# Kernel tuning notes

Hardware: AMD Instinct MI355X
Metric: run time of the kernel (lower is better)

The kernel has to match this reference:

```python
import jax, jax.numpy as jnp
import numpy as np

N_HEAD = 16
LN_EPS = 1e-5


def _layernorm(x, g, b):
    mu = jnp.mean(x, axis=-1, keepdims=True)
    var = jnp.mean(jnp.square(x - mu), axis=-1, keepdims=True)
    return (x - mu) * jax.lax.rsqrt(var + LN_EPS) * g + b


def setup_inputs() -> dict:
    key = jax.random.key(0)
    ks = jax.random.split(key, 8)
    B, T, C = 2, 2048, 1024
    Dff = 4 * C
    s = 0.02
    return {
        "x": jax.random.normal(ks[0], (B, T, C), jnp.float32),
        "wq": jax.random.normal(ks[1], (C, C), jnp.float32) * s,
        "wk": jax.random.normal(ks[2], (C, C), jnp.float32) * s,
        "wv": jax.random.normal(ks[3], (C, C), jnp.float32) * s,
        "w_proj": jax.random.normal(ks[4], (C, C), jnp.float32) * s,
        "b_proj": jnp.zeros((C,), jnp.float32),
        "w1": jax.random.normal(ks[5], (C, Dff), jnp.float32) * s,
        "b1": jnp.zeros((Dff,), jnp.float32),
        "w2": jax.random.normal(ks[6], (Dff, C), jnp.float32) * s,
        "b2": jnp.zeros((C,), jnp.float32),
        "g1": jnp.ones((C,), jnp.float32),
        "be1": jnp.zeros((C,), jnp.float32),
        "g2": jnp.ones((C,), jnp.float32),
        "be2": jnp.zeros((C,), jnp.float32),
    }


def reference(x, wq, wk, wv, w_proj, b_proj, w1, b1, w2, b2, g1, be1, g2, be2):
    B, T, C = x.shape
    H = N_HEAD
    hd = C // H
    # QKV projections (all heads folded into one matmul each), -> [B,H,T,hd]
    q = (x @ wq).reshape(B, T, H, hd).transpose(0, 2, 1, 3)
    k = (x @ wk).reshape(B, T, H, hd).transpose(0, 2, 1, 3)
    v = (x @ wv).reshape(B, T, H, hd).transpose(0, 2, 1, 3)
    # scaled causal attention; scale = head_size ** -0.5 as in torch source
    scores = jnp.einsum("bhqd,bhkd->bhqk", q, k) * (hd ** -0.5)
    causal = jnp.tril(jnp.ones((T, T), bool))
    scores = jnp.where(causal, scores, jnp.finfo(scores.dtype).min)
    wei = jax.nn.softmax(scores, axis=-1)
    attn = jnp.einsum("bhqk,bhkd->bhqd", wei, v)  # [B,H,T,hd]
    attn = attn.transpose(0, 2, 1, 3).reshape(B, T, C)
    y = attn @ w_proj + b_proj
    # post-LN residuals as in Block.forward
    x = _layernorm(x + y, g1, be1)
    y = jnp.maximum(x @ w1 + b1, 0.0) @ w2 + b2
    x = _layernorm(x + y, g2, be2)
    return x
```

## Files before the change

### kernel.cpp

```cpp
#include <hip/hip_runtime.h>
#include <hip/hip_bf16.h>


typedef __attribute__((ext_vector_type(8))) short bf16x8;
typedef __attribute__((ext_vector_type(4))) float f32x4;
typedef __attribute__((ext_vector_type(4))) short short4v;

__device__ inline short f2bf(float f) {
    __hip_bfloat16 h = __float2bfloat16(f);
    return *reinterpret_cast<short*>(&h);
}
__device__ inline float bf2f(short s) {
    union { unsigned u; float f; } c;
    c.u = ((unsigned)(unsigned short)s) << 16;
    return c.f;
}


__global__ __launch_bounds__(256) void convert_f2b(const float* __restrict__ in,
                                                   short* __restrict__ out, int n4) {
    int i = blockIdx.x * 256 + threadIdx.x;
    if (i < n4) {
        float4 v = *(const float4*)(in + (size_t)i * 4);
        short4v o = { f2bf(v.x), f2bf(v.y), f2bf(v.z), f2bf(v.w) };
        *(short4v*)(out + (size_t)i * 4) = o;
    }
}

__global__ __launch_bounds__(256) void transpose4_f2b(const float* __restrict__ s0,
                                                      const float* __restrict__ s1,
                                                      const float* __restrict__ s2,
                                                      const float* __restrict__ s3,
                                                      short* __restrict__ d0,
                                                      short* __restrict__ d1,
                                                      short* __restrict__ d2,
                                                      short* __restrict__ d3,
                                                      float scale0) {
    __shared__ short tile[32][33];
    const int z = blockIdx.z;
    const float* in = z == 0 ? s0 : z == 1 ? s1 : z == 2 ? s2 : s3;
    short* out = z == 0 ? d0 : z == 1 ? d1 : z == 2 ? d2 : d3;
    const float scale = z == 0 ? scale0 : 1.0f;
    int c0 = blockIdx.x * 32, r0 = blockIdx.y * 32;
    int tx = threadIdx.x, ty = threadIdx.y;
    for (int i = ty; i < 32; i += 8)
        tile[i][tx] = f2bf(in[(size_t)(r0 + i) * 1024 + c0 + tx] * scale);
    __syncthreads();
    for (int i = ty; i < 32; i += 8)
        out[(size_t)(c0 + i) * 1024 + r0 + tx] = tile[tx][i];
}

__global__ __launch_bounds__(256) void transpose_f2b(const float* __restrict__ in,
                                                     short* __restrict__ out, int R, int C,
                                                     float scale) {
    __shared__ short tile[32][33];
    int c0 = blockIdx.x * 32, r0 = blockIdx.y * 32;
    int tx = threadIdx.x, ty = threadIdx.y;
    for (int i = ty; i < 32; i += 8)
        tile[i][tx] = f2bf(in[(size_t)(r0 + i) * C + c0 + tx] * scale);
    __syncthreads();
    for (int i = ty; i < 32; i += 8)
        out[(size_t)(c0 + i) * R + r0 + tx] = tile[tx][i];
}

template <int BN, int BIAS, int RELU, int OUTBF>
__device__ __forceinline__ void gemm_core(const short* __restrict__ A,
                                          const short* __restrict__ BT,
                                          const float* __restrict__ bias,
                                          void* __restrict__ Cout,
                                          int N, int K, int lda, int ldb,
                                          int gx, int w,
                                          short* As, short* Bs, bool addbias) {
    constexpr int NI = BN / 32;
    const int tid = threadIdx.x;
    const int wid = tid >> 6;
    const int lane = tid & 63;
    const int wr = wid >> 1, wc = wid & 1;
    const int row0 = (w % gx) * 128;
    const int col0 = (w / gx) * BN;
    const int lr = lane & 15;
    const int lk = (lane >> 4) * 8;
    const int sr = lane >> 3;
    const int scs = ((lane & 7) * 8) ^ (sr * 8);
    const int rsw = (lr & 7) * 8;

    f32x4 acc[4][NI] = {};
    for (int k = 0; k < K; k += 64) {
#pragma unroll
        for (int c = 0; c < 4; ++c) {
            const int ch = wid + c * 4;
            const short* ga = A + (size_t)(row0 + ch * 8 + sr) * lda + k + scs;
            __builtin_amdgcn_global_load_lds(
                (const __attribute__((address_space(1))) unsigned int*)ga,
                (__attribute__((address_space(3))) unsigned int*)(As + ch * 512), 16, 0, 0);
        }
#pragma unroll
        for (int c = 0; c < BN / 32; ++c) {
            const int ch = wid + c * 4;
            const short* gb = BT + (size_t)(col0 + ch * 8 + sr) * ldb + k + scs;
            __builtin_amdgcn_global_load_lds(
                (const __attribute__((address_space(1))) unsigned int*)gb,
                (__attribute__((address_space(3))) unsigned int*)(Bs + ch * 512), 16, 0, 0);
        }
        __syncthreads();
#pragma unroll
        for (int kk = 0; kk < 64; kk += 32) {
            const int cof = (kk + lk) ^ rsw;
            bf16x8 a[4], b[NI];
#pragma unroll
            for (int m = 0; m < 4; ++m)
                a[m] = *(const bf16x8*)(As + (wr * 64 + m * 16 + lr) * 64 + cof);
#pragma unroll
            for (int n = 0; n < NI; ++n)
                b[n] = *(const bf16x8*)(Bs + (wc * (BN / 2) + n * 16 + lr) * 64 + cof);
#pragma unroll
            for (int m = 0; m < 4; ++m)
#pragma unroll
                for (int n = 0; n < NI; ++n)
                    acc[m][n] = __builtin_amdgcn_mfma_f32_16x16x32_bf16(a[m], b[n], acc[m][n], 0, 0, 0);
        }
        __syncthreads();
    }
#pragma unroll
    for (int m = 0; m < 4; ++m) {
        int row = row0 + wr * 64 + m * 16 + (lane >> 4) * 4;
#pragma unroll
        for (int n = 0; n < NI; ++n) {
            int col = col0 + wc * (BN / 2) + n * 16 + lr;
            float bv = (BIAS && addbias) ? bias[col] : 0.0f;
#pragma unroll
            for (int r = 0; r < 4; ++r) {
                float v = acc[m][n][r] + bv;
                if (RELU) v = fmaxf(v, 0.0f);
                if (OUTBF)
                    ((short*)Cout)[(size_t)(row + r) * N + col] = f2bf(v);
                else
                    ((float*)Cout)[(size_t)(row + r) * N + col] = v;
            }
        }
    }
}

template <int BN, int BIAS, int RELU, int OUTBF>
__global__ __launch_bounds__(256) void gemm_bt(const short* __restrict__ A,
                                               const short* __restrict__ BT,
                                               const float* __restrict__ bias,
                                               void* __restrict__ Cout,
                                               int N, int K, int lda, int ldb,
                                               void* __restrict__ Cout2) {
    __shared__ short As[128 * 64];
    __shared__ short Bs[BN * 64];
    const int kz = blockIdx.z;
    if (kz) { A += K; BT += K; Cout = Cout2; }
    const int gx = gridDim.x;
    int flat = blockIdx.x + gx * blockIdx.y;
    const int nwg = gx * gridDim.y;
    int w = flat;
    if ((nwg & 7) == 0) {
        const int q = nwg >> 3;
        w = (flat & 7) * q + (flat >> 3);
    }
    gemm_core<BN, BIAS, RELU, OUTBF>(A, BT, bias, Cout, N, K, lda, ldb, gx, w, As, Bs, kz == 0);
}

__global__ __launch_bounds__(256) void gemm_qkv_vt(const short* __restrict__ x_bf,
                                                   const short* __restrict__ wqkT,
                                                   const short* __restrict__ wvT,
                                                   short* __restrict__ qk,
                                                   short* __restrict__ Vt) {
    __shared__ short As[128 * 64];
    __shared__ short Bs[128 * 64];
    int flat = blockIdx.x;
    if (flat < 512) {
        const int w = (flat & 7) * 64 + (flat >> 3);
        gemm_core<128, 0, 0, 1>(x_bf, wqkT, nullptr, qk, 2048, 1024, 1024, 1024, 32, w, As, Bs, false);
    } else {
        flat -= 512;
        const int w = (flat & 7) * 32 + (flat >> 3);
        gemm_core<128, 0, 0, 1>(wvT, x_bf, nullptr, Vt, 4096, 1024, 1024, 1024, 8, w, As, Bs, false);
    }
}

#define ATT_T 2048
#define ATT_QKS 2048
#define ATT_BT 4096

#define LOADK(KF, KB)                                                                     \
    do {                                                                                  \
        const int k0_ = (KB) * 64;                                                        \
        _Pragma("unroll") for (int t = 0; t < 4; ++t) {                                   \
            const size_t krow_ = (size_t)(b * ATT_T + k0_ + 16 * t + lr) * ATT_QKS + h * 64; \
            KF[t][0] = *(const bf16x8*)(Km + krow_ + g * 8);                              \
            KF[t][1] = *(const bf16x8*)(Km + krow_ + 32 + g * 8);                         \
        }                                                                                 \
    } while (0)

#define LOADV(VF, KB)                                                                     \
    do {                                                                                  \
        const int k0_ = (KB) * 64;                                                        \
        _Pragma("unroll") for (int n = 0; n < 4; ++n)                                     \
            _Pragma("unroll") for (int ks = 0; ks < 2; ++ks)                              \
                VF[n][ks] = *(const bf16x8*)(Vt + (size_t)(h * 64 + n * 16 + lr) * ATT_BT + \
                                             b * ATT_T + k0_ + ks * 32 + g * 8);          \
    } while (0)

#define COMPUTE(KF, VF, KB)                                                               \
    do {                                                                                  \
        const int k0_ = (KB) * 64;                                                        \
        const bool edge_ = (KB) == nfull;                                                 \
        _Pragma("unroll") for (int qs = 0; qs < 2; ++qs) {                                \
            f32x4 st[4];                                                                  \
            __builtin_amdgcn_s_setprio(1);                                                \
            _Pragma("unroll") for (int t = 0; t < 4; ++t) {                               \
                f32x4 s = {};                                                             \
                s = __builtin_amdgcn_mfma_f32_16x16x32_bf16(KF[t][0], aq[qs][0], s, 0, 0, 0); \
                s = __builtin_amdgcn_mfma_f32_16x16x32_bf16(KF[t][1], aq[qs][1], s, 0, 0, 0); \
                st[t] = s;                                                                \
            }                                                                             \
            __builtin_amdgcn_s_setprio(0);                                                \
            float rs = 0.0f;                                                              \
            _Pragma("unroll") for (int t = 0; t < 4; ++t) {                               \
                short4v pw;                                                               \
                _Pragma("unroll") for (int r = 0; r < 4; ++r) {                           \
                    float val = st[t][r];                                                 \
                    if (edge_ && (k0_ + 16 * t + g * 4 + r > qrow[qs])) val = -3e38f;     \
                    float p = exp2f(val);                                                 \
                    rs += p;                                                              \
                    pw[r] = f2bf(p);                                                      \
                }                                                                         \
                *(short4v*)(&Plds[wid][qs][lr][16 * t + g * 4]) = pw;                     \
            }                                                                             \
            rs += __shfl_xor(rs, 16);                                                     \
            rs += __shfl_xor(rs, 32);                                                     \
            lrun[qs] += rs;                                                               \
        }                                                                                 \
        asm volatile("s_waitcnt lgkmcnt(0)" ::: "memory");                                \
        __builtin_amdgcn_sched_barrier(0);                                                \
        __builtin_amdgcn_s_setprio(1);                                                    \
        _Pragma("unroll") for (int qs = 0; qs < 2; ++qs)                                  \
            _Pragma("unroll") for (int ks = 0; ks < 2; ++ks) {                            \
                bf16x8 pf = *(const bf16x8*)(&Plds[wid][qs][lr][ks * 32 + g * 8]);        \
                _Pragma("unroll") for (int n = 0; n < 4; ++n)                             \
                    O[qs][n] = __builtin_amdgcn_mfma_f32_16x16x32_bf16(VF[n][ks], pf, O[qs][n], 0, 0, 0); \
            }                                                                             \
        __builtin_amdgcn_s_setprio(0);                                                    \
    } while (0)

__global__ __launch_bounds__(128) void flash_attn(const short* __restrict__ Q,
                                                  const short* __restrict__ Km,
                                                  const short* __restrict__ Vt,
                                                  short* __restrict__ Oout) {
    const int f = blockIdx.x;
    const int wid = threadIdx.x >> 6;
    const int lane = threadIdx.x & 63;
    const int lr = lane & 15;
    const int g = lane >> 4;
    const int xcd = f & 7;
    const int k = f >> 3;
    const int bh = xcd * 4 + (k & 3);
    const int b = bh >> 4;
    const int h = bh & 15;
    const int pair = (k >> 2) * 2 + wid;

    __shared__ __align__(16) short Plds[2][2][16][72];

#pragma unroll 1
    for (int job = 0; job < 2; ++job) {
        const int s = job ? (63 - pair) : pair;
        const int q0 = s << 5;
        const int qrow[2] = { q0 + lr, q0 + 16 + lr };
        const int nfull = s >> 1;

        bf16x8 aq[2][2];
#pragma unroll
        for (int qs = 0; qs < 2; ++qs)
#pragma unroll
            for (int ds = 0; ds < 2; ++ds)
                aq[qs][ds] = *(const bf16x8*)(Q + (size_t)(b * ATT_T + q0 + qs * 16 + lr) * ATT_QKS +
                                              h * 64 + ds * 32 + g * 8);

        f32x4 O[2][4] = {};
        float lrun[2] = { 0.0f, 0.0f };

        bf16x8 kfA[4][2], kfB[4][2], vfA[4][2], vfB[4][2];
        LOADK(kfA, 0);
        LOADV(vfA, 0);
        int kb = 0;
        while (true) {
            if (kb < nfull) { LOADK(kfB, kb + 1); LOADV(vfB, kb + 1); }
            COMPUTE(kfA, vfA, kb);
            ++kb;
            if (kb > nfull) break;
            if (kb < nfull) { LOADK(kfA, kb + 1); LOADV(vfA, kb + 1); }
            COMPUTE(kfB, vfB, kb);
            ++kb;
            if (kb > nfull) break;
        }

#pragma unroll
        for (int qs = 0; qs < 2; ++qs) {
            const float inv = 1.0f / lrun[qs];
#pragma unroll
            for (int n = 0; n < 4; ++n) {
                short4v ov;
#pragma unroll
                for (int r = 0; r < 4; ++r) ov[r] = f2bf(O[qs][n][r] * inv);
                *(short4v*)(Oout + (size_t)(b * ATT_T + q0 + qs * 16 + lr) * 1024 +
                            h * 64 + n * 16 + g * 4) = ov;
            }
        }
    }
}

__global__ __launch_bounds__(256) void resid_ln(const float* __restrict__ x,
                                                const short* __restrict__ y,
                                                const short* __restrict__ yb,
                                                const float* __restrict__ g,
                                                const float* __restrict__ be,
                                                float* __restrict__ of,
                                                short* __restrict__ ob) {
    const int row = blockIdx.x;
    const int tid = threadIdx.x;
    const size_t base = (size_t)row * 1024 + tid * 4;
    float4 xv = *(const float4*)(x + base);
    short4v yv = *(const short4v*)(y + base);
    float h0 = xv.x + bf2f(yv[0]), h1 = xv.y + bf2f(yv[1]);
    float h2 = xv.z + bf2f(yv[2]), h3 = xv.w + bf2f(yv[3]);
    if (yb) {
        short4v bv2 = *(const short4v*)(yb + base);
        h0 += bf2f(bv2[0]); h1 += bf2f(bv2[1]); h2 += bf2f(bv2[2]); h3 += bf2f(bv2[3]);
    }
    float s = h0 + h1 + h2 + h3;
    float ss = h0 * h0 + h1 * h1 + h2 * h2 + h3 * h3;
#pragma unroll
    for (int d = 1; d < 64; d <<= 1) {
        s += __shfl_xor(s, d);
        ss += __shfl_xor(ss, d);
    }
    __shared__ float as_[4], ass_[4];
    if ((tid & 63) == 0) { as_[tid >> 6] = s; ass_[tid >> 6] = ss; }
    __syncthreads();
    s = as_[0] + as_[1] + as_[2] + as_[3];
    ss = ass_[0] + ass_[1] + ass_[2] + ass_[3];
    const float mu = s * (1.0f / 1024.0f);
    const float var = ss * (1.0f / 1024.0f) - mu * mu;
    const float rstd = rsqrtf(var + 1e-5f);
    float4 gv = *(const float4*)(g + tid * 4);
    float4 bv = *(const float4*)(be + tid * 4);
    float o0 = (h0 - mu) * rstd * gv.x + bv.x;
    float o1 = (h1 - mu) * rstd * gv.y + bv.y;
    float o2 = (h2 - mu) * rstd * gv.z + bv.z;
    float o3 = (h3 - mu) * rstd * gv.w + bv.w;
    float4 ov = { o0, o1, o2, o3 };
    *(float4*)(of + base) = ov;
    if (ob) {
        short4v obv = { f2bf(o0), f2bf(o1), f2bf(o2), f2bf(o3) };
        *(short4v*)(ob + base) = obv;
    }
}


extern "C" void kernel_launch(void* const* d_in, const int* in_sizes, int n_in,
                              void* d_out, int out_size, void* d_ws, size_t ws_size,
                              hipStream_t stream) {
    const float* x = (const float*)d_in[0];
    const float* wq = (const float*)d_in[1];
    const float* wk = (const float*)d_in[2];
    const float* wv = (const float*)d_in[3];
    const float* wp = (const float*)d_in[4];
    const float* bproj = (const float*)d_in[5];
    const float* w1 = (const float*)d_in[6];
    const float* b1 = (const float*)d_in[7];
    const float* w2 = (const float*)d_in[8];
    const float* b2 = (const float*)d_in[9];
    const float* g1 = (const float*)d_in[10];
    const float* be1 = (const float*)d_in[11];
    const float* g2 = (const float*)d_in[12];
    const float* be2 = (const float*)d_in[13];

    char* ws = (char*)d_ws;
    const size_t MB = 1024 * 1024;
    short* x_bf = (short*)(ws + 0);
    short* wqkT = (short*)(ws + 8 * MB);
    short* wqT = wqkT;
    short* wkT = (short*)(ws + 10 * MB);
    short* wvT = (short*)(ws + 12 * MB);
    short* w1T = (short*)(ws + 16 * MB);
    short* w2T = (short*)(ws + 24 * MB);
    short* qk  = (short*)(ws + 32 * MB);
    short* wpT = (short*)(ws + 48 * MB);
    short* Vt  = (short*)(ws + 56 * MB);
    short* hbf = (short*)(ws + 32 * MB);
    short* attn = (short*)(ws + 64 * MB);
    short* x1bf = (short*)(ws + 64 * MB);
    short* y1a = (short*)(ws + 72 * MB);
    short* y1b = (short*)(ws + 0);
    short* y2a = (short*)(ws + 72 * MB);
    short* y2b = (short*)(ws + 0);
    float* x1f = (float*)(ws + 88 * MB);

    dim3 blk(256);
    dim3 tb(32, 8);
    const float SC = 0.125f * 1.44269504089f;

    convert_f2b<<<dim3(4096), blk, 0, stream>>>(x, x_bf, 4096 * 1024 / 4);
    transpose4_f2b<<<dim3(32, 32, 4), tb, 0, stream>>>(wq, wk, wv, wp, wqT, wkT, wvT, wpT, SC);
    transpose_f2b<<<dim3(128, 32), tb, 0, stream>>>(w1, w1T, 1024, 4096, 1.0f);
    transpose_f2b<<<dim3(32, 128), tb, 0, stream>>>(w2, w2T, 4096, 1024, 1.0f);

    gemm_qkv_vt<<<dim3(768), blk, 0, stream>>>(x_bf, wqkT, wvT, qk, Vt);
    flash_attn<<<dim3(512), dim3(128), 0, stream>>>(qk, qk + 1024, Vt, attn);
    gemm_bt<64, 1, 0, 1><<<dim3(32, 16, 2), blk, 0, stream>>>(attn, wpT, bproj, y1a,
                                                              1024, 512, 1024, 1024, y1b);
    resid_ln<<<dim3(4096), blk, 0, stream>>>(x, y1a, y1b, g1, be1, x1f, x1bf);
    gemm_bt<128, 1, 1, 1><<<dim3(32, 32), blk, 0, stream>>>(x1bf, w1T, b1, hbf,
                                                            4096, 1024, 1024, 1024, nullptr);
    gemm_bt<64, 1, 0, 1><<<dim3(32, 16, 2), blk, 0, stream>>>(hbf, w2T, b2, y2a,
                                                              1024, 2048, 4096, 4096, y2b);
    resid_ln<<<dim3(4096), blk, 0, stream>>>(x1f, y2a, y2b, g2, be2, (float*)d_out, nullptr);
}
```

Baseline: 295.4 us.

## Merge prep conversion kernels into one launch and single-buffer V in attention

The x conversion and all the weight transpose/convert kernels are folded into one mega_prep launch that dispatches on block index, removing three kernel launches and their gaps. Separately, the flash attention loop stops double-buffering V fragments: V is now loaded right before each compute step, and only K stays prefetched. The V change cuts register pressure and may raise occupancy, but it exposes V load latency in each iteration.

After: 283.8 us. 3.9% less time.

```diff
diff --git a/kernel.cpp b/kernel.cpp
--- a/kernel.cpp
+++ b/kernel.cpp
@@ -16,46 +16,57 @@
     return c.f;
 }
 
-
-__global__ __launch_bounds__(256) void convert_f2b(const float* __restrict__ in,
-                                                   short* __restrict__ out, int n4) {
-    int i = blockIdx.x * 256 + threadIdx.x;
-    if (i < n4) {
-        float4 v = *(const float4*)(in + (size_t)i * 4);
+__global__ __launch_bounds__(256) void mega_prep(const float* __restrict__ x,
+                                                 short* __restrict__ x_bf,
+                                                 const float* __restrict__ wq,
+                                                 const float* __restrict__ wk,
+                                                 const float* __restrict__ wv,
+                                                 const float* __restrict__ wp,
+                                                 short* __restrict__ wqT,
+                                                 short* __restrict__ wkT,
+                                                 short* __restrict__ wvT,
+                                                 short* __restrict__ wpT,
+                                                 const float* __restrict__ w1,
+                                                 short* __restrict__ w1T,
+                                                 const float* __restrict__ w2,
+                                                 short* __restrict__ w2T,
+                                                 float scaleq) {
+    const int blk = blockIdx.x;
+    const int tid = threadIdx.x;
+    if (blk < 4096) {
+        const int i = blk * 256 + tid;
+        float4 v = *(const float4*)(x + (size_t)i * 4);
         short4v o = { f2bf(v.x), f2bf(v.y), f2bf(v.z), f2bf(v.w) };
-        *(short4v*)(out + (size_t)i * 4) = o;
-    }
-}
-
-__global__ __launch_bounds__(256) void transpose4_f2b(const float* __restrict__ s0,
-                                                      const float* __restrict__ s1,
-                                                      const float* __restrict__ s2,
-                                                      const float* __restrict__ s3,
-                                                      short* __restrict__ d0,
-                                                      short* __restrict__ d1,
-                                                      short* __restrict__ d2,
-                                                      short* __restrict__ d3,
-                                                      float scale0) {
+        *(short4v*)(x_bf + (size_t)i * 4) = o;
+        return;
+    }
     __shared__ short tile[32][33];
-    const int z = blockIdx.z;
-    const float* in = z == 0 ? s0 : z == 1 ? s1 : z == 2 ? s2 : s3;
-    short* out = z == 0 ? d0 : z == 1 ? d1 : z == 2 ? d2 : d3;
-    const float scale = z == 0 ? scale0 : 1.0f;
-    int c0 = blockIdx.x * 32, r0 = blockIdx.y * 32;
-    int tx = threadIdx.x, ty = threadIdx.y;
-    for (int i = ty; i < 32; i += 8)
-        tile[i][tx] = f2bf(in[(size_t)(r0 + i) * 1024 + c0 + tx] * scale);
-    __syncthreads();
-    for (int i = ty; i < 32; i += 8)
-        out[(size_t)(c0 + i) * 1024 + r0 + tx] = tile[tx][i];
-}
-
-__global__ __launch_bounds__(256) void transpose_f2b(const float* __restrict__ in,
-                                                     short* __restrict__ out, int R, int C,
-                                                     float scale) {
-    __shared__ short tile[32][33];
-    int c0 = blockIdx.x * 32, r0 = blockIdx.y * 32;
-    int tx = threadIdx.x, ty = threadIdx.y;
+    const int tx = tid & 31, ty = tid >> 5;
+    const float* in;
+    short* out;
+    int R, C, bx, by;
+    float scale = 1.0f;
+    if (blk < 8192) {
+        const int b2 = blk - 4096;
+        const int z = b2 >> 10;
+        const int rem = b2 & 1023;
+        bx = rem & 31; by = rem >> 5;
+        R = 1024; C = 1024;
+        in = z == 0 ? wq : z == 1 ? wk : z == 2 ? wv : wp;
+        out = z == 0 ? wqT : z == 1 ? wkT : z == 2 ? wvT : wpT;
+        if (z == 0) scale = scaleq;
+    } else if (blk < 12288) {
+        const int rem = blk - 8192;
+        bx = rem & 127; by = rem >> 7;
+        R = 1024; C = 4096;
+        in = w1; out = w1T;
+    } else {
+        const int rem = blk - 12288;
+        bx = rem & 31; by = rem >> 5;
+        R = 4096; C = 1024;
+        in = w2; out = w2T;
+    }
+    const int c0 = bx * 32, r0 = by * 32;
     for (int i = ty; i < 32; i += 8)
         tile[i][tx] = f2bf(in[(size_t)(r0 + i) * C + c0 + tx] * scale);
     __syncthreads();
@@ -282,17 +293,18 @@
         f32x4 O[2][4] = {};
         float lrun[2] = { 0.0f, 0.0f };
 
-        bf16x8 kfA[4][2], kfB[4][2], vfA[4][2], vfB[4][2];
+        bf16x8 kfA[4][2], kfB[4][2], vf[4][2];
         LOADK(kfA, 0);
-        LOADV(vfA, 0);
         int kb = 0;
         while (true) {
-            if (kb < nfull) { LOADK(kfB, kb + 1); LOADV(vfB, kb + 1); }
-            COMPUTE(kfA, vfA, kb);
+            LOADV(vf, kb);
+            if (kb < nfull) LOADK(kfB, kb + 1);
+            COMPUTE(kfA, vf, kb);
             ++kb;
             if (kb > nfull) break;
-            if (kb < nfull) { LOADK(kfA, kb + 1); LOADV(vfA, kb + 1); }
-            COMPUTE(kfB, vfB, kb);
+            LOADV(vf, kb);
+            if (kb < nfull) LOADK(kfA, kb + 1);
+            COMPUTE(kfB, vf, kb);
             ++kb;
             if (kb > nfull) break;
         }
@@ -400,14 +412,11 @@
     float* x1f = (float*)(ws + 88 * MB);
 
     dim3 blk(256);
-    dim3 tb(32, 8);
     const float SC = 0.125f * 1.44269504089f;
 
-    convert_f2b<<<dim3(4096), blk, 0, stream>>>(x, x_bf, 4096 * 1024 / 4);
-    transpose4_f2b<<<dim3(32, 32, 4), tb, 0, stream>>>(wq, wk, wv, wp, wqT, wkT, wvT, wpT, SC);
-    transpose_f2b<<<dim3(128, 32), tb, 0, stream>>>(w1, w1T, 1024, 4096, 1.0f);
-    transpose_f2b<<<dim3(32, 128), tb, 0, stream>>>(w2, w2T, 4096, 1024, 1.0f);
-
+    mega_prep<<<dim3(16384), blk, 0, stream>>>(x, x_bf, wq, wk, wv, wp,
+                                               wqT, wkT, wvT, wpT,
+                                               w1, w1T, w2, w2T, SC);
     gemm_qkv_vt<<<dim3(768), blk, 0, stream>>>(x_bf, wqkT, wvT, qk, Vt);
     flash_attn<<<dim3(512), dim3(128), 0, stream>>>(qk, qk + 1024, Vt, attn);
     gemm_bt<64, 1, 0, 1><<<dim3(32, 16, 2), blk, 0, stream>>>(attn, wpT, bproj, y1a,
```
